# Optimization experiments

Measured on AMD Instinct MI355X. Metric: run time of the kernel, lower is better.

The kernel has to match this reference:

```python
import jax, jax.numpy as jnp
import numpy as np

PI = 3.141592653589793
M = 1500.0; IZ = 2250.0; LF = 1.2; LR = 1.6; CF = 80000.0; CR = 80000.0
TAU_A = 0.1; TAU_DELTA = 0.1
MAX_STEER = 30.0 * PI / 180.0
MAX_ACCEL = 3.0; MIN_ACCEL = -6.0
MU = 0.9; G = 9.81
L = LF + LR
FY_F_MAX = MU * M * G * (LR / L)
FY_R_MAX = MU * M * G * (LF / L)
V_EFF_MIN = 20.0 / 3.6
DT = 0.1
DT_INT = 0.01
B = 4194304


def setup_inputs() -> dict:
    key = jax.random.key(0)
    k1, k2 = jax.random.split(key)
    init_state = jax.random.normal(k1, (B, 9), dtype=jnp.float32)
    action = jax.random.normal(k2, (B, 2), dtype=jnp.float32)
    return {"init_state": init_state, "action": action}


def _substep(state, a_ref, h):
    # state: (B, 9) = [x, y, psi, v, a, delta, beta, r, delta_ref]
    x, y, psi, v, a, delta, beta, r, delta_ref = (state[:, i] for i in range(9))
    a_dot = (a_ref - a) / TAU_A
    delta_dot = (delta_ref - delta) / TAU_DELTA
    v_eff = jnp.maximum(v, V_EFF_MIN)
    alpha_f = beta + LF * r / v_eff - delta
    alpha_r = beta - LR * r / v_eff
    F_yf = jnp.clip(-CF * alpha_f, -FY_F_MAX, FY_F_MAX)
    F_yr = jnp.clip(-CR * alpha_r, -FY_R_MAX, FY_R_MAX)
    beta_dot = (F_yf + F_yr) / (M * v_eff) - r
    r_dot = (LF * F_yf - LR * F_yr) / IZ
    psi_eff = psi + beta
    new_state = jnp.stack([
        x + v * jnp.cos(psi_eff) * h,
        y + v * jnp.sin(psi_eff) * h,
        psi + r * h,
        jnp.maximum(v + a * h, 0.0),
        a + a_dot * h,
        jnp.clip(delta + delta_dot * h, -MAX_STEER, MAX_STEER),
        beta + beta_dot * h,
        r + r_dot * h,
        delta_ref,
    ], axis=1)
    return new_state


def _forward(init_state, action):
    # reset(): postprocess clamps
    s = init_state
    s = s.at[:, 3].set(jnp.maximum(s[:, 3], 0.0))
    s = s.at[:, 5].set(jnp.clip(s[:, 5], -MAX_STEER, MAX_STEER))
    s = s.at[:, 8].set(jnp.clip(s[:, 8], -MAX_STEER, MAX_STEER))
    # step(): ZOH action, clamp, overwrite delta_ref
    a_ref = jnp.clip(action[:, 0], MIN_ACCEL, MAX_ACCEL)
    delta_ref_cmd = jnp.clip(action[:, 1], -MAX_STEER, MAX_STEER)
    s = s.at[:, 8].set(delta_ref_cmd)
    # replicate torch's Python float substep bookkeeping exactly
    n_full = int(DT // DT_INT)
    dt_rem = DT - n_full * DT_INT
    h = jnp.float32(DT_INT)

    def body(st, _):
        return _substep(st, a_ref, h), None

    s, _ = jax.lax.scan(body, s, None, length=n_full)
    if dt_rem > 1e-12:
        s = _substep(s, a_ref, jnp.float32(dt_rem))
    return s


def reference(init_state, action):
    return _forward(init_state, action)
```

## Files before the change

kernel.cpp:

```cpp
#include <hip/hip_runtime.h>
#include <math.h>


typedef float v2f __attribute__((ext_vector_type(2)));
typedef float f4  __attribute__((ext_vector_type(4)));

__device__ __forceinline__ float med3(float x, float lo, float hi) {
    return __builtin_amdgcn_fmed3f(x, lo, hi);
}
__device__ __forceinline__ v2f vfma2(v2f a, v2f b, v2f c) {
    return __builtin_elementwise_fma(a, b, c);
}

__global__ __launch_bounds__(256, 4) void bicycle_kernel(
    const float* __restrict__ state_in,
    const float* __restrict__ action_in,
    float* __restrict__ out)
{
    constexpr float MAX_STEER = (float)(30.0 * 3.141592653589793 / 180.0);
    constexpr float V_EFF_MIN = (float)(20.0 / 3.6);
    constexpr float FY_F_MAX  = (float)(0.9 * 1500.0 * 9.81 * (1.6 / 2.8));
    constexpr float FY_R_MAX  = (float)(0.9 * 1500.0 * 9.81 * (1.2 / 2.8));

    __shared__ float smem[4 * 2304];

    const int tid  = threadIdx.x;
    const int wid  = tid >> 6;
    const int lane = tid & 63;
    float* ws  = smem + wid * 2304;
    f4*    ws4 = (f4*)ws;

    const size_t W = (size_t)blockIdx.x * 4 + wid;

    f4     pk[9];
    float2 actp[4];

    auto loadp = [&](int t) {
        const size_t R = (W * 4 + (size_t)t) * 256;
        const f4* g4 = (const f4*)(state_in + R * 9);
#pragma unroll
        for (int i = 0; i < 9; ++i) pk[i] = g4[lane + 64 * i];
        const float2* a2 = (const float2*)action_in + R;
#pragma unroll
        for (int j = 0; j < 4; ++j) actp[j] = a2[lane + 64 * j];
    };
    auto commit = [&]() {
#pragma unroll
        for (int i = 0; i < 9; ++i) ws4[lane + 64 * i] = pk[i];
    };

    loadp(0);
    commit();

#pragma unroll
    for (int t = 0; t < 4; ++t) {
        v2f a_ref[2], d_ref[2];
#pragma unroll
        for (int p = 0; p < 2; ++p) {
            a_ref[p] = (v2f){med3(actp[2 * p + 0].x, -6.0f, 3.0f),
                             med3(actp[2 * p + 1].x, -6.0f, 3.0f)};
            d_ref[p] = (v2f){med3(actp[2 * p + 0].y, -MAX_STEER, MAX_STEER),
                             med3(actp[2 * p + 1].y, -MAX_STEER, MAX_STEER)};
        }
        if (t < 3) loadp(t + 1);

        v2f x[2], y[2], psi[2], v[2], a[2], delta[2], beta[2], r[2], cs[2], sn[2];
#pragma unroll
        for (int p = 0; p < 2; ++p) {
            const int r0 = (lane + 64 * (2 * p + 0)) * 9;
            const int r1 = (lane + 64 * (2 * p + 1)) * 9;
            x[p]     = (v2f){ws[r0 + 0], ws[r1 + 0]};
            y[p]     = (v2f){ws[r0 + 1], ws[r1 + 1]};
            psi[p]   = (v2f){ws[r0 + 2], ws[r1 + 2]};
            v[p]     = (v2f){fmaxf(ws[r0 + 3], 0.0f), fmaxf(ws[r1 + 3], 0.0f)};
            a[p]     = (v2f){ws[r0 + 4], ws[r1 + 4]};
            delta[p] = (v2f){med3(ws[r0 + 5], -MAX_STEER, MAX_STEER),
                             med3(ws[r1 + 5], -MAX_STEER, MAX_STEER)};
            beta[p]  = (v2f){ws[r0 + 6], ws[r1 + 6]};
            r[p]     = (v2f){ws[r0 + 7], ws[r1 + 7]};
            float s0, c0, s1, c1;
            __sincosf(psi[p].x + beta[p].x, &s0, &c0);
            __sincosf(psi[p].y + beta[p].y, &s1, &c1);
            cs[p] = (v2f){c0, c1};
            sn[p] = (v2f){s0, s1};
        }

#pragma unroll
        for (int k = 0; k < 10; ++k) {
#pragma unroll
            for (int p = 0; p < 2; ++p) {
                v2f v_eff = {fmaxf(v[p].x, V_EFF_MIN), fmaxf(v[p].y, V_EFF_MIN)};
                v2f inv_v = {__builtin_amdgcn_rcpf(v_eff.x), __builtin_amdgcn_rcpf(v_eff.y)};
                v2f tt = r[p] * inv_v;
                v2f alpha_f = vfma2((v2f)(1.2f), tt, beta[p]) - delta[p];
                v2f alpha_r = vfma2((v2f)(-1.6f), tt, beta[p]);
                v2f Ff_raw = alpha_f * -80000.0f;
                v2f Fr_raw = alpha_r * -80000.0f;
                v2f F_yf = {med3(Ff_raw.x, -FY_F_MAX, FY_F_MAX), med3(Ff_raw.y, -FY_F_MAX, FY_F_MAX)};
                v2f F_yr = {med3(Fr_raw.x, -FY_R_MAX, FY_R_MAX), med3(Fr_raw.y, -FY_R_MAX, FY_R_MAX)};
                v2f beta_dot = vfma2(F_yf + F_yr, inv_v * (1.0f / 1500.0f), -r[p]);
                v2f r_dot = vfma2((v2f)(1.2f), F_yf, F_yr * -1.6f) * (1.0f / 2250.0f);

                v2f vh = v[p] * 0.01f;
                x[p] = vfma2(vh, cs[p], x[p]);
                y[p] = vfma2(vh, sn[p], y[p]);

                v2f d  = (r[p] + beta_dot) * 0.01f;
                v2f cd = vfma2(d * d, (v2f)(-0.5f), (v2f)(1.0f));
                v2f cs_n = vfma2(cs[p], cd, -(sn[p] * d));
                v2f sn_n = vfma2(sn[p], cd, cs[p] * d);

                v2f v_new = vfma2(a[p], (v2f)(0.01f), v[p]);
                v_new = (v2f){fmaxf(v_new.x, 0.0f), fmaxf(v_new.y, 0.0f)};
                psi[p]  = vfma2(r[p], (v2f)(0.01f), psi[p]);
                a[p]    = vfma2(a_ref[p] - a[p], (v2f)(0.1f), a[p]);
                v2f dlt = vfma2(d_ref[p] - delta[p], (v2f)(0.1f), delta[p]);
                delta[p] = (v2f){med3(dlt.x, -MAX_STEER, MAX_STEER), med3(dlt.y, -MAX_STEER, MAX_STEER)};
                beta[p] = vfma2(beta_dot, (v2f)(0.01f), beta[p]);
                r[p]    = vfma2(r_dot, (v2f)(0.01f), r[p]);
                v[p] = v_new;
                cs[p] = cs_n;
                sn[p] = sn_n;
            }
        }

#pragma unroll
        for (int p = 0; p < 2; ++p) {
            const int r0 = (lane + 64 * (2 * p + 0)) * 9;
            const int r1 = (lane + 64 * (2 * p + 1)) * 9;
            ws[r0 + 0] = x[p].x;     ws[r1 + 0] = x[p].y;
            ws[r0 + 1] = y[p].x;     ws[r1 + 1] = y[p].y;
            ws[r0 + 2] = psi[p].x;   ws[r1 + 2] = psi[p].y;
            ws[r0 + 3] = v[p].x;     ws[r1 + 3] = v[p].y;
            ws[r0 + 4] = a[p].x;     ws[r1 + 4] = a[p].y;
            ws[r0 + 5] = delta[p].x; ws[r1 + 5] = delta[p].y;
            ws[r0 + 6] = beta[p].x;  ws[r1 + 6] = beta[p].y;
            ws[r0 + 7] = r[p].x;     ws[r1 + 7] = r[p].y;
            ws[r0 + 8] = d_ref[p].x; ws[r1 + 8] = d_ref[p].y;
        }

        f4 st[9];
#pragma unroll
        for (int i = 0; i < 9; ++i) st[i] = ws4[lane + 64 * i];
        const size_t R = (W * 4 + (size_t)t) * 256;
        f4* o4 = (f4*)(out + R * 9);
#pragma unroll
        for (int i = 0; i < 9; ++i)
            __builtin_nontemporal_store(st[i], &o4[lane + 64 * i]);

        if (t < 3) commit();
    }
}

extern "C" void kernel_launch(void* const* d_in, const int* in_sizes, int n_in,
                              void* d_out, int out_size, void* d_ws, size_t ws_size,
                              hipStream_t stream) {
    const float* state  = (const float*)d_in[0];
    const float* action = (const float*)d_in[1];
    float* out = (float*)d_out;
    const int rows = in_sizes[0] / 9;
    const int grid = rows / 4096;
    bicycle_kernel<<<grid, 256, 0, stream>>>(state, action, out);
}
```

Measured before the change: 56.08 us.

## Use closed-form a/delta decay, move prefetch later, and use buffer stores

```diff
diff --git a/kernel.cpp b/kernel.cpp
--- a/kernel.cpp
+++ b/kernel.cpp
@@ -4,6 +4,13 @@
 
 typedef float v2f __attribute__((ext_vector_type(2)));
 typedef float f4  __attribute__((ext_vector_type(4)));
+typedef unsigned int u4 __attribute__((ext_vector_type(4)));
+
+#if __has_builtin(__builtin_amdgcn_make_buffer_rsrc) && __has_builtin(__builtin_amdgcn_raw_buffer_store_b128)
+#define USE_BUFFER_STORE 1
+#else
+#define USE_BUFFER_STORE 0
+#endif
 
 __device__ __forceinline__ float med3(float x, float lo, float hi) {
     return __builtin_amdgcn_fmed3f(x, lo, hi);
@@ -11,16 +18,26 @@
 __device__ __forceinline__ v2f vfma2(v2f a, v2f b, v2f c) {
     return __builtin_elementwise_fma(a, b, c);
 }
+__device__ __forceinline__ v2f vmax2(v2f a, v2f b) {
+    return __builtin_elementwise_max(a, b);
+}
+__device__ __forceinline__ v2f vmin2(v2f a, v2f b) {
+    return __builtin_elementwise_min(a, b);
+}
 
 __global__ __launch_bounds__(256, 4) void bicycle_kernel(
     const float* __restrict__ state_in,
     const float* __restrict__ action_in,
-    float* __restrict__ out)
+    float* __restrict__ out,
+    unsigned int out_bytes)
 {
     constexpr float MAX_STEER = (float)(30.0 * 3.141592653589793 / 180.0);
     constexpr float V_EFF_MIN = (float)(20.0 / 3.6);
     constexpr float FY_F_MAX  = (float)(0.9 * 1500.0 * 9.81 * (1.6 / 2.8));
     constexpr float FY_R_MAX  = (float)(0.9 * 1500.0 * 9.81 * (1.2 / 2.8));
+    constexpr float CK[11] = {1.0f, 0.9f, 0.81f, 0.729f, 0.6561f, 0.59049f,
+                              0.531441f, 0.4782969f, 0.43046721f,
+                              0.387420489f, 0.3486784401f};
 
     __shared__ float smem[4 * 2304];
 
@@ -31,6 +48,12 @@
     f4*    ws4 = (f4*)ws;
 
     const size_t W = (size_t)blockIdx.x * 4 + wid;
+
+#if USE_BUFFER_STORE
+    __amdgpu_buffer_rsrc_t srd = __builtin_amdgcn_make_buffer_rsrc(
+        (void*)out, (short)0, (int)out_bytes,
+        0x00020000);
+#endif
 
     f4     pk[9];
     float2 actp[4];
@@ -62,9 +85,8 @@
             d_ref[p] = (v2f){med3(actp[2 * p + 0].y, -MAX_STEER, MAX_STEER),
                              med3(actp[2 * p + 1].y, -MAX_STEER, MAX_STEER)};
         }
-        if (t < 3) loadp(t + 1);
 
-        v2f x[2], y[2], psi[2], v[2], a[2], delta[2], beta[2], r[2], cs[2], sn[2];
+        v2f x[2], y[2], psi[2], v[2], beta[2], r[2], cs[2], sn[2], da[2], dd[2];
 #pragma unroll
         for (int p = 0; p < 2; ++p) {
             const int r0 = (lane + 64 * (2 * p + 0)) * 9;
@@ -72,12 +94,14 @@
             x[p]     = (v2f){ws[r0 + 0], ws[r1 + 0]};
             y[p]     = (v2f){ws[r0 + 1], ws[r1 + 1]};
             psi[p]   = (v2f){ws[r0 + 2], ws[r1 + 2]};
-            v[p]     = (v2f){fmaxf(ws[r0 + 3], 0.0f), fmaxf(ws[r1 + 3], 0.0f)};
-            a[p]     = (v2f){ws[r0 + 4], ws[r1 + 4]};
-            delta[p] = (v2f){med3(ws[r0 + 5], -MAX_STEER, MAX_STEER),
+            v[p]     = vmax2((v2f){ws[r0 + 3], ws[r1 + 3]}, (v2f)(0.0f));
+            v2f a0   = (v2f){ws[r0 + 4], ws[r1 + 4]};
+            v2f dl0  = (v2f){med3(ws[r0 + 5], -MAX_STEER, MAX_STEER),
                              med3(ws[r1 + 5], -MAX_STEER, MAX_STEER)};
             beta[p]  = (v2f){ws[r0 + 6], ws[r1 + 6]};
             r[p]     = (v2f){ws[r0 + 7], ws[r1 + 7]};
+            da[p] = a0  - a_ref[p];
+            dd[p] = dl0 - d_ref[p];
             float s0, c0, s1, c1;
             __sincosf(psi[p].x + beta[p].x, &s0, &c0);
             __sincosf(psi[p].y + beta[p].y, &s1, &c1);
@@ -85,19 +109,21 @@
             sn[p] = (v2f){s0, s1};
         }
 
+        if (t < 3) loadp(t + 1);
+
 #pragma unroll
         for (int k = 0; k < 10; ++k) {
 #pragma unroll
             for (int p = 0; p < 2; ++p) {
-                v2f v_eff = {fmaxf(v[p].x, V_EFF_MIN), fmaxf(v[p].y, V_EFF_MIN)};
+                v2f ak = vfma2((v2f)(CK[k]), da[p], a_ref[p]);
+                v2f dk = vfma2((v2f)(CK[k]), dd[p], d_ref[p]);
+                v2f v_eff = vmax2(v[p], (v2f)(V_EFF_MIN));
                 v2f inv_v = {__builtin_amdgcn_rcpf(v_eff.x), __builtin_amdgcn_rcpf(v_eff.y)};
                 v2f tt = r[p] * inv_v;
-                v2f alpha_f = vfma2((v2f)(1.2f), tt, beta[p]) - delta[p];
+                v2f alpha_f = vfma2((v2f)(1.2f), tt, beta[p]) - dk;
                 v2f alpha_r = vfma2((v2f)(-1.6f), tt, beta[p]);
-                v2f Ff_raw = alpha_f * -80000.0f;
-                v2f Fr_raw = alpha_r * -80000.0f;
-                v2f F_yf = {med3(Ff_raw.x, -FY_F_MAX, FY_F_MAX), med3(Ff_raw.y, -FY_F_MAX, FY_F_MAX)};
-                v2f F_yr = {med3(Fr_raw.x, -FY_R_MAX, FY_R_MAX), med3(Fr_raw.y, -FY_R_MAX, FY_R_MAX)};
+                v2f F_yf = vmin2(vmax2(alpha_f * -80000.0f, (v2f)(-FY_F_MAX)), (v2f)(FY_F_MAX));
+                v2f F_yr = vmin2(vmax2(alpha_r * -80000.0f, (v2f)(-FY_R_MAX)), (v2f)(FY_R_MAX));
                 v2f beta_dot = vfma2(F_yf + F_yr, inv_v * (1.0f / 1500.0f), -r[p]);
                 v2f r_dot = vfma2((v2f)(1.2f), F_yf, F_yr * -1.6f) * (1.0f / 2250.0f);
 
@@ -110,15 +136,10 @@
                 v2f cs_n = vfma2(cs[p], cd, -(sn[p] * d));
                 v2f sn_n = vfma2(sn[p], cd, cs[p] * d);
 
-                v2f v_new = vfma2(a[p], (v2f)(0.01f), v[p]);
-                v_new = (v2f){fmaxf(v_new.x, 0.0f), fmaxf(v_new.y, 0.0f)};
-                psi[p]  = vfma2(r[p], (v2f)(0.01f), psi[p]);
-                a[p]    = vfma2(a_ref[p] - a[p], (v2f)(0.1f), a[p]);
-                v2f dlt = vfma2(d_ref[p] - delta[p], (v2f)(0.1f), delta[p]);
-                delta[p] = (v2f){med3(dlt.x, -MAX_STEER, MAX_STEER), med3(dlt.y, -MAX_STEER, MAX_STEER)};
+                v[p]   = vmax2(vfma2(ak, (v2f)(0.01f), v[p]), (v2f)(0.0f));
+                psi[p] = vfma2(r[p], (v2f)(0.01f), psi[p]);
                 beta[p] = vfma2(beta_dot, (v2f)(0.01f), beta[p]);
-                r[p]    = vfma2(r_dot, (v2f)(0.01f), r[p]);
-                v[p] = v_new;
+                r[p]   = vfma2(r_dot, (v2f)(0.01f), r[p]);
                 cs[p] = cs_n;
                 sn[p] = sn_n;
             }
@@ -126,14 +147,16 @@
 
 #pragma unroll
         for (int p = 0; p < 2; ++p) {
+            v2f a10 = vfma2((v2f)(CK[10]), da[p], a_ref[p]);
+            v2f d10 = vfma2((v2f)(CK[10]), dd[p], d_ref[p]);
             const int r0 = (lane + 64 * (2 * p + 0)) * 9;
             const int r1 = (lane + 64 * (2 * p + 1)) * 9;
             ws[r0 + 0] = x[p].x;     ws[r1 + 0] = x[p].y;
             ws[r0 + 1] = y[p].x;     ws[r1 + 1] = y[p].y;
             ws[r0 + 2] = psi[p].x;   ws[r1 + 2] = psi[p].y;
             ws[r0 + 3] = v[p].x;     ws[r1 + 3] = v[p].y;
-            ws[r0 + 4] = a[p].x;     ws[r1 + 4] = a[p].y;
-            ws[r0 + 5] = delta[p].x; ws[r1 + 5] = delta[p].y;
+            ws[r0 + 4] = a10.x;      ws[r1 + 4] = a10.y;
+            ws[r0 + 5] = d10.x;      ws[r1 + 5] = d10.y;
             ws[r0 + 6] = beta[p].x;  ws[r1 + 6] = beta[p].y;
             ws[r0 + 7] = r[p].x;     ws[r1 + 7] = r[p].y;
             ws[r0 + 8] = d_ref[p].x; ws[r1 + 8] = d_ref[p].y;
@@ -142,13 +165,22 @@
         f4 st[9];
 #pragma unroll
         for (int i = 0; i < 9; ++i) st[i] = ws4[lane + 64 * i];
+
+        if (t < 3) commit();
+
         const size_t R = (W * 4 + (size_t)t) * 256;
+#if USE_BUFFER_STORE
+        const int voff = (int)(R * 36) + lane * 16;
+#pragma unroll
+        for (int i = 0; i < 9; ++i)
+            __builtin_amdgcn_raw_buffer_store_b128(
+                __builtin_bit_cast(u4, st[i]), srd, voff + i * 1024, 0, 19);
+#else
         f4* o4 = (f4*)(out + R * 9);
 #pragma unroll
         for (int i = 0; i < 9; ++i)
             __builtin_nontemporal_store(st[i], &o4[lane + 64 * i]);
-
-        if (t < 3) commit();
+#endif
     }
 }
 
@@ -160,5 +192,6 @@
     float* out = (float*)d_out;
     const int rows = in_sizes[0] / 9;
     const int grid = rows / 4096;
-    bicycle_kernel<<<grid, 256, 0, stream>>>(state, action, out);
+    bicycle_kernel<<<grid, 256, 0, stream>>>(state, action, out,
+                                             (unsigned int)out_size * 4u);
 }
```

Measured after the change: 55.93 us. Within noise of the previous version (-0.3%).
